# Kernel optimization log

Measured on AMD Instinct MI355X. Metric: run time of the kernel, lower is better.

## Reference

```python
import jax, jax.numpy as jnp
import numpy as np

N = 100000          # nodes
E = 1600000         # edges
F = 128             # input features
H = 128             # hidden_channels
G = 64              # graphs in batch


def setup_inputs() -> dict:
    key = jax.random.key(0)
    ks = jax.random.split(key, 16)
    x = jax.random.normal(ks[0], (N, F), dtype=jnp.float32)
    edge_index = jax.random.randint(ks[1], (2, E), 0, N, dtype=jnp.int32)
    batch = jnp.sort(jax.random.randint(ks[2], (N,), 0, G, dtype=jnp.int32))

    def glorot(k, fan_in, fan_out):
        s = jnp.sqrt(6.0 / (fan_in + fan_out)).astype(jnp.float32)
        return jax.random.uniform(k, (fan_in, fan_out), jnp.float32, -s, s)

    return {
        "x": x, "edge_index": edge_index, "batch": batch,
        "W1": glorot(ks[3], F, H),       "b1": jnp.zeros((H,), jnp.float32),
        "W2": glorot(ks[4], H, H),       "b2": jnp.zeros((H,), jnp.float32),
        "W3": glorot(ks[5], H, 2 * H),   "b3": jnp.zeros((2 * H,), jnp.float32),
        "W4": glorot(ks[6], 2 * H, H),   "b4": jnp.zeros((H,), jnp.float32),
        "Wl": glorot(ks[7], F, H),       "bl": jnp.zeros((H,), jnp.float32),
    }


def _gcn_conv(x, W, b, src, dst, deg_inv_sqrt):
    # PyG GCNConv: add self-loops, symmetric normalization D^-1/2 (A+I) D^-1/2
    h = x @ W                                  # [N, out]
    norm = deg_inv_sqrt[src] * deg_inv_sqrt[dst]      # [E]
    msg = h[src] * norm[:, None]               # gather + scale, [E, out]
    agg = jax.ops.segment_sum(msg, dst, num_segments=N)
    agg = agg + h * (deg_inv_sqrt * deg_inv_sqrt)[:, None]  # self-loop term (norm = 1/deg)
    return agg + b


def reference(x, edge_index, batch, W1, b1, W2, b2, W3, b3, W4, b4, Wl, bl):
    src, dst = edge_index[0], edge_index[1]
    # degree (incl. self-loop) from dst, as in PyG gcn_norm
    deg = jax.ops.segment_sum(jnp.ones((E,), jnp.float32), dst, num_segments=N) + 1.0
    deg_inv_sqrt = jax.lax.rsqrt(deg)

    identity = x
    x = jax.nn.relu(_gcn_conv(x, W1, b1, src, dst, deg_inv_sqrt))
    x = jax.nn.relu(_gcn_conv(x, W2, b2, src, dst, deg_inv_sqrt))
    x = jax.nn.relu(_gcn_conv(x, W3, b3, src, dst, deg_inv_sqrt))
    x = _gcn_conv(x, W4, b4, src, dst, deg_inv_sqrt)
    x = x + (identity @ Wl + bl)

    # global_mean_pool over graph ids
    sums = jax.ops.segment_sum(x, batch, num_segments=G)
    cnts = jax.ops.segment_sum(jnp.ones((N,), jnp.float32), batch, num_segments=G)
    return sums / jnp.maximum(cnts, 1.0)[:, None]
```

## Files before the change

kernel.cpp:

```cpp
#include <hip/hip_runtime.h>

#define NN 100000
#define EE 1600000
#define GG 64
#define PBLK 391
#define PCHUNK 4096
#define NBUCK 196

typedef __attribute__((ext_vector_type(8))) short short8v;
typedef __attribute__((ext_vector_type(4))) float f32x4;

__device__ __forceinline__ unsigned short f2bf(float f) {
    unsigned u = __float_as_uint(f);
    u = (u + 0x7FFFu + ((u >> 16) & 1)) >> 16;
    return (unsigned short)u;
}
__device__ __forceinline__ float bf2f(unsigned short s) {
    return __uint_as_float((unsigned)s << 16);
}

__global__ __launch_bounds__(256) void partitionA_kernel(const int* __restrict__ src,
                                                         const int* __restrict__ dst,
                                                         int* __restrict__ cnt,
                                                         int* __restrict__ ghist,
                                                         int* __restrict__ gboff,
                                                         int2* __restrict__ stage) {
    __shared__ int hist[NBUCK];
    __shared__ int boff[NBUCK];
    __shared__ int bcur[NBUCK];
    int b = blockIdx.x, t = threadIdx.x;
    int e0 = b * PCHUNK;
    int n = EE - e0;
    if (n > PCHUNK) n = PCHUNK;
    for (int i = t; i < NBUCK; i += 256) { hist[i] = 0; bcur[i] = 0; }
    __syncthreads();
    for (int i = t; i < n; i += 256) {
        int d = dst[e0 + i];
        atomicAdd(&cnt[d], 1);
        atomicAdd(&hist[d >> 9], 1);
    }
    __syncthreads();
    if (t == 0) {
        int run = 0;
        for (int k = 0; k < NBUCK; ++k) { boff[k] = run; run += hist[k]; }
    }
    __syncthreads();
    for (int i = t; i < n; i += 256) {
        int d = dst[e0 + i];
        int sv = src[e0 + i];
        int k = d >> 9;
        int p = boff[k] + atomicAdd(&bcur[k], 1);
        stage[(size_t)b * PCHUNK + p] = make_int2(sv, d);
    }
    for (int k = t; k < NBUCK; k += 256) {
        ghist[b * NBUCK + k] = hist[k];
        gboff[b * NBUCK + k] = boff[k];
    }
}

__global__ __launch_bounds__(256) void dis_kernel(const int* __restrict__ cnt,
                                                  float* __restrict__ dis) {
    int i = blockIdx.x * 256 + threadIdx.x;
    if (i < NN) dis[i] = rsqrtf((float)cnt[i] + 1.0f);
}

#define SCAN_EPB 1024
__global__ __launch_bounds__(256) void scan_block_kernel(const int* __restrict__ in,
                                                         int* __restrict__ out,
                                                         int* __restrict__ bsums) {
    __shared__ int sd[256];
    int t = threadIdx.x;
    int base = blockIdx.x * SCAN_EPB + t * 4;
    int v[4];
#pragma unroll
    for (int j = 0; j < 4; ++j) v[j] = (base + j < NN) ? in[base + j] : 0;
    int s = v[0] + v[1] + v[2] + v[3];
    sd[t] = s;
    __syncthreads();
    for (int off = 1; off < 256; off <<= 1) {
        int add = (t >= off) ? sd[t - off] : 0;
        __syncthreads();
        sd[t] += add;
        __syncthreads();
    }
    int ex = sd[t] - s;
    int run = ex;
#pragma unroll
    for (int j = 0; j < 4; ++j) {
        if (base + j < NN) out[base + j] = run;
        run += v[j];
    }
    if (t == 255) bsums[blockIdx.x] = sd[255];
}

__global__ void scan_sums_kernel(int* __restrict__ bsums, int nb) {
    if (threadIdx.x == 0 && blockIdx.x == 0) {
        int run = 0;
        for (int i = 0; i < nb; ++i) {
            int v = bsums[i];
            bsums[i] = run;
            run += v;
        }
    }
}

__global__ __launch_bounds__(256) void scan_add_kernel(int* __restrict__ rs,
                                                       const int* __restrict__ bsums,
                                                       int* __restrict__ cursor) {
    int i = blockIdx.x * 256 + threadIdx.x;
    if (i < NN) {
        int v = rs[i] + bsums[i >> 10];
        rs[i] = v;
        cursor[i] = v;
    }
    if (i == 0) rs[NN] = EE;
}

__global__ __launch_bounds__(256) void scatterC_kernel(const int2* __restrict__ stage,
                                                       const int* __restrict__ ghist,
                                                       const int* __restrict__ gboff,
                                                       int* __restrict__ cursor,
                                                       int* __restrict__ csr) {
    int k = blockIdx.x;
    for (int b = threadIdx.x; b < PBLK; b += 256) {
        int c_ = ghist[b * NBUCK + k];
        size_t base = (size_t)b * PCHUNK + gboff[b * NBUCK + k];
        for (int i = 0; i < c_; ++i) {
            int2 e = stage[base + i];
            int p = atomicAdd(&cursor[e.y], 1);
            csr[p] = e.x;
        }
    }
}

__global__ __launch_bounds__(256) void cvt_kernel(const float* __restrict__ x,
                                                  const float* __restrict__ dis,
                                                  unsigned short* __restrict__ xb) {
    size_t i = ((size_t)blockIdx.x * 256 + threadIdx.x) * 8;
    float d = dis[i >> 7];
    float4 a = *(const float4*)(x + i);
    float4 b = *(const float4*)(x + i + 4);
    short8v v;
    v[0] = (short)f2bf(a.x * d); v[1] = (short)f2bf(a.y * d);
    v[2] = (short)f2bf(a.z * d); v[3] = (short)f2bf(a.w * d);
    v[4] = (short)f2bf(b.x * d); v[5] = (short)f2bf(b.y * d);
    v[6] = (short)f2bf(b.z * d); v[7] = (short)f2bf(b.w * d);
    *(short8v*)(xb + i) = v;
}

template <int K, int M>
__global__ __launch_bounds__(64) void packw_kernel(const float* __restrict__ W,
                                                   unsigned short* __restrict__ Wp) {
    const int NKS = K / 32;
    int ct = blockIdx.x / NKS, ks = blockIdx.x % NKS;
    int lane = threadIdx.x;
    int col = ct * 16 + (lane & 15);
    int kb = ks * 32 + (lane >> 4) * 8;
    unsigned short* o = Wp + ((size_t)(ct * NKS + ks) * 64 + lane) * 16;
#pragma unroll
    for (int i = 0; i < 8; ++i) {
        float f = W[(size_t)(kb + i) * M + col];
        unsigned short h = f2bf(f);
        unsigned short l = f2bf(f - bf2f(h));
        o[i] = h;
        o[8 + i] = l;
    }
}

template <int K, int M, int RT, bool ASPLIT, bool RELU, bool BIAS, bool ACCUM, bool DSCALE>
__global__ __launch_bounds__(256) void gemm_kernel(const void* __restrict__ Ain,
                                                   const unsigned short* __restrict__ Wp,
                                                   const float* __restrict__ bias,
                                                   const float* __restrict__ dis,
                                                   void* __restrict__ out) {
    const int NKS = K / 32;
    int tid = threadIdx.x;
    int wave = tid >> 6, lane = tid & 63;
    int r0 = blockIdx.x * (RT * 64) + wave * (RT * 16);

    short8v ah[RT][NKS];
    short8v al[ASPLIT ? RT : 1][ASPLIT ? NKS : 1];
#pragma unroll
    for (int t = 0; t < RT; ++t) {
        int ra = r0 + t * 16 + (lane & 15);
        if (ra > NN - 1) ra = NN - 1;
        if (ASPLIT) {
            const float* A = (const float*)Ain;
#pragma unroll
            for (int ks = 0; ks < NKS; ++ks) {
                const float* p = A + (size_t)ra * K + ks * 32 + (lane >> 4) * 8;
                float4 v0 = *(const float4*)p;
                float4 v1 = *(const float4*)(p + 4);
                float f[8] = {v0.x, v0.y, v0.z, v0.w, v1.x, v1.y, v1.z, v1.w};
#pragma unroll
                for (int i = 0; i < 8; ++i) {
                    unsigned short h = f2bf(f[i]);
                    ah[t][ks][i] = (short)h;
                    al[t][ks][i] = (short)f2bf(f[i] - bf2f(h));
                }
            }
        } else {
            const unsigned short* A = (const unsigned short*)Ain;
#pragma unroll
            for (int ks = 0; ks < NKS; ++ks)
                ah[t][ks] = *(const short8v*)(A + (size_t)ra * K + ks * 32 + (lane >> 4) * 8);
        }
    }

    float dsc[RT][4];
#pragma unroll
    for (int t = 0; t < RT; ++t)
#pragma unroll
        for (int i = 0; i < 4; ++i) {
            int row = r0 + t * 16 + (lane >> 4) * 4 + i;
            dsc[t][i] = (DSCALE && row < NN) ? dis[row] : 1.f;
        }

#pragma unroll
    for (int ct = 0; ct < 8; ++ct) {
        int ctg = blockIdx.y * 8 + ct;
        int col = ctg * 16 + (lane & 15);
        float bv = BIAS ? bias[col] : 0.f;
        f32x4 acc[RT];
#pragma unroll
        for (int t = 0; t < RT; ++t) {
            acc[t][0] = bv; acc[t][1] = bv; acc[t][2] = bv; acc[t][3] = bv;
        }
#pragma unroll
        for (int ks = 0; ks < NKS; ++ks) {
            const short8v* pW = (const short8v*)Wp + ((size_t)(ctg * NKS + ks) * 64 + lane) * 2;
            short8v bh = pW[0], blo = pW[1];
#pragma unroll
            for (int t = 0; t < RT; ++t) {
                acc[t] = __builtin_amdgcn_mfma_f32_16x16x32_bf16(ah[t][ks], bh, acc[t], 0, 0, 0);
                acc[t] = __builtin_amdgcn_mfma_f32_16x16x32_bf16(ah[t][ks], blo, acc[t], 0, 0, 0);
                if (ASPLIT)
                    acc[t] = __builtin_amdgcn_mfma_f32_16x16x32_bf16(al[t][ks], bh, acc[t], 0, 0, 0);
            }
        }
#pragma unroll
        for (int t = 0; t < RT; ++t)
#pragma unroll
            for (int i = 0; i < 4; ++i) {
                int row = r0 + t * 16 + (lane >> 4) * 4 + i;
                if (row >= NN) continue;
                float v = acc[t][i];
                if (RELU) v = fmaxf(v, 0.f);
                if (ACCUM) {
                    ((float*)out)[(size_t)row * M + col] += v;
                } else {
                    ((unsigned short*)out)[(size_t)row * M + col] = f2bf(v * dsc[t][i]);
                }
            }
    }
}

template <int OUTMODE>
__global__ __launch_bounds__(256) void aggb_kernel(const unsigned short* __restrict__ h,
                                                   const float* __restrict__ dis,
                                                   const int* __restrict__ csr,
                                                   const int* __restrict__ rs,
                                                   const float* __restrict__ bias,
                                                   void* __restrict__ out) {
    int node = blockIdx.x * 4 + (threadIdx.x >> 6);
    int lane = threadIdx.x & 63;
    if (node >= NN) return;
    int c = lane & 15;
    int s = lane >> 4;
    int beg = rs[node], end = rs[node + 1];
    const uint4* hb = (const uint4*)h;
    float acc[8] = {};
    for (int e0 = beg; e0 < end; e0 += 32) {
        uint4 v[8];
#pragma unroll
        for (int j = 0; j < 8; ++j) {
            v[j] = make_uint4(0u, 0u, 0u, 0u);
            int ej = e0 + j * 4 + s;
            if (ej < end) v[j] = hb[(size_t)csr[ej] * 16 + c];
        }
#pragma unroll
        for (int j = 0; j < 8; ++j) {
            acc[0] += __uint_as_float(v[j].x << 16);
            acc[1] += __uint_as_float(v[j].x & 0xFFFF0000u);
            acc[2] += __uint_as_float(v[j].y << 16);
            acc[3] += __uint_as_float(v[j].y & 0xFFFF0000u);
            acc[4] += __uint_as_float(v[j].z << 16);
            acc[5] += __uint_as_float(v[j].z & 0xFFFF0000u);
            acc[6] += __uint_as_float(v[j].w << 16);
            acc[7] += __uint_as_float(v[j].w & 0xFFFF0000u);
        }
    }
#pragma unroll
    for (int i = 0; i < 8; ++i) {
        acc[i] += __shfl_xor(acc[i], 16, 64);
        acc[i] += __shfl_xor(acc[i], 32, 64);
    }
    if (s == 0) {
        float d = dis[node];
        uint4 us = hb[(size_t)node * 16 + c];
        float sf[8];
        sf[0] = __uint_as_float(us.x << 16); sf[1] = __uint_as_float(us.x & 0xFFFF0000u);
        sf[2] = __uint_as_float(us.y << 16); sf[3] = __uint_as_float(us.y & 0xFFFF0000u);
        sf[4] = __uint_as_float(us.z << 16); sf[5] = __uint_as_float(us.z & 0xFFFF0000u);
        sf[6] = __uint_as_float(us.w << 16); sf[7] = __uint_as_float(us.w & 0xFFFF0000u);
        float r[8];
#pragma unroll
        for (int i = 0; i < 8; ++i) r[i] = d * (acc[i] + sf[i]);
        if (OUTMODE == 0) {
            uint4 o;
            o.x = (unsigned)f2bf(r[0]) | ((unsigned)f2bf(r[1]) << 16);
            o.y = (unsigned)f2bf(r[2]) | ((unsigned)f2bf(r[3]) << 16);
            o.z = (unsigned)f2bf(r[4]) | ((unsigned)f2bf(r[5]) << 16);
            o.w = (unsigned)f2bf(r[6]) | ((unsigned)f2bf(r[7]) << 16);
            ((uint4*)out)[(size_t)node * 16 + c] = o;
        } else {
#pragma unroll
            for (int i = 0; i < 8; ++i) r[i] += bias[c * 8 + i];
            float4 o0 = make_float4(r[0], r[1], r[2], r[3]);
            float4 o1 = make_float4(r[4], r[5], r[6], r[7]);
            float* O = (float*)out + (size_t)node * 128 + c * 8;
            *(float4*)O = o0;
            *(float4*)(O + 4) = o1;
        }
    }
}

__global__ __launch_bounds__(128) void pool_partial_kernel(const float* __restrict__ y,
                                                           const int* __restrict__ batch,
                                                           float* __restrict__ P) {
    int c = threadIdx.x;
    int chunk = (NN + gridDim.x - 1) / gridDim.x;
    int n0 = blockIdx.x * chunk;
    int n1 = n0 + chunk;
    if (n1 > NN) n1 = NN;
    if (n0 >= NN) return;
    int curg = batch[n0];
    float acc = 0.f;
    for (int n = n0; n < n1; ++n) {
        int g = batch[n];
        if (g != curg) {
            atomicAdd(&P[curg * 128 + c], acc);
            acc = 0.f;
            curg = g;
        }
        acc += y[(size_t)n * 128 + c];
    }
    atomicAdd(&P[curg * 128 + c], acc);
}

__global__ __launch_bounds__(128) void pool_final_kernel(const float* __restrict__ P,
                                                         const int* __restrict__ batch,
                                                         float* __restrict__ out) {
    int g = blockIdx.x, c = threadIdx.x;
    int lo = 0, hi = NN;
    while (lo < hi) {
        int m = (lo + hi) >> 1;
        if (batch[m] < g) lo = m + 1;
        else hi = m;
    }
    int start = lo;
    int lo2 = start, hi2 = NN;
    while (lo2 < hi2) {
        int m = (lo2 + hi2) >> 1;
        if (batch[m] < g + 1) lo2 = m + 1;
        else hi2 = m;
    }
    float cntg = (float)(lo2 - start);
    out[g * 128 + c] = P[g * 128 + c] / fmaxf(cntg, 1.f);
}

extern "C" void kernel_launch(void* const* d_in, const int* in_sizes, int n_in,
                              void* d_out, int out_size, void* d_ws, size_t ws_size,
                              hipStream_t stream) {
    const float* x = (const float*)d_in[0];
    const int* ei = (const int*)d_in[1];
    const int* batch = (const int*)d_in[2];
    const float* W1 = (const float*)d_in[3];
    const float* b1 = (const float*)d_in[4];
    const float* W2 = (const float*)d_in[5];
    const float* b2 = (const float*)d_in[6];
    const float* W3 = (const float*)d_in[7];
    const float* b3 = (const float*)d_in[8];
    const float* W4 = (const float*)d_in[9];
    const float* b4 = (const float*)d_in[10];
    const float* Wl = (const float*)d_in[11];
    const float* bl = (const float*)d_in[12];
    float* out = (float*)d_out;

    char* p = (char*)d_ws;
    auto alloc = [&](size_t bytes) {
        void* r = (void*)p;
        p += (bytes + 255) & ~(size_t)255;
        return r;
    };
    int* cnt = (int*)alloc((size_t)NN * 4);
    int* rs = (int*)alloc((size_t)(NN + 1) * 4);
    int* cursor = (int*)alloc((size_t)NN * 4);
    float* dis = (float*)alloc((size_t)NN * 4);
    const int NB = (NN + SCAN_EPB - 1) / SCAN_EPB;
    int* bsums = (int*)alloc((size_t)NB * 4);
    int* csr = (int*)alloc((size_t)EE * 4);
    int* ghist = (int*)alloc((size_t)PBLK * NBUCK * 4);
    int* gboff = (int*)alloc((size_t)PBLK * NBUCK * 4);
    unsigned short* xb = (unsigned short*)alloc((size_t)NN * 128 * 2);
    unsigned short* AG = (unsigned short*)alloc((size_t)NN * 128 * 2);
    unsigned short* GM = (unsigned short*)alloc((size_t)NN * 128 * 2);
    unsigned short* H3 = (unsigned short*)alloc((size_t)NN * 256 * 2);
    float* Y = (float*)alloc((size_t)NN * 128 * 4);
    unsigned short* W1p = (unsigned short*)alloc(8 * 4 * 64 * 16 * 2);
    unsigned short* W2p = (unsigned short*)alloc(8 * 4 * 64 * 16 * 2);
    unsigned short* W3p = (unsigned short*)alloc(16 * 4 * 64 * 16 * 2);
    unsigned short* W4p = (unsigned short*)alloc(8 * 8 * 64 * 16 * 2);
    unsigned short* Wlp = (unsigned short*)alloc(8 * 4 * 64 * 16 * 2);
    float* P = (float*)alloc((size_t)GG * 128 * 4);
    int2* stage = (int2*)Y;

    const int* src = ei;
    const int* dst = ei + EE;

    hipMemsetAsync(cnt, 0, (size_t)NN * 4, stream);
    hipMemsetAsync(P, 0, (size_t)GG * 128 * 4, stream);

    partitionA_kernel<<<PBLK, 256, 0, stream>>>(src, dst, cnt, ghist, gboff, stage);
    dis_kernel<<<(NN + 255) / 256, 256, 0, stream>>>(cnt, dis);
    cvt_kernel<<<(NN * 128) / (256 * 8), 256, 0, stream>>>(x, dis, xb);
    scan_block_kernel<<<NB, 256, 0, stream>>>(cnt, rs, bsums);
    scan_sums_kernel<<<1, 64, 0, stream>>>(bsums, NB);
    scan_add_kernel<<<(NN + 255) / 256, 256, 0, stream>>>(rs, bsums, cursor);
    scatterC_kernel<<<NBUCK, 256, 0, stream>>>(stage, ghist, gboff, cursor, csr);

    packw_kernel<128, 128><<<8 * 4, 64, 0, stream>>>(W1, W1p);
    packw_kernel<128, 128><<<8 * 4, 64, 0, stream>>>(W2, W2p);
    packw_kernel<128, 256><<<16 * 4, 64, 0, stream>>>(W3, W3p);
    packw_kernel<256, 128><<<8 * 8, 64, 0, stream>>>(W4, W4p);
    packw_kernel<128, 128><<<8 * 4, 64, 0, stream>>>(Wl, Wlp);

    const int AGG_GRID = (NN + 3) / 4;
    const int GX4 = (NN + 255) / 256;
    const int GX2 = (NN + 127) / 128;

    aggb_kernel<0><<<AGG_GRID, 256, 0, stream>>>(xb, dis, csr, rs, nullptr, AG);
    gemm_kernel<128, 128, 4, false, true, true, false, true><<<dim3(GX4, 1), 256, 0, stream>>>(AG, W1p, b1, dis, GM);
    aggb_kernel<0><<<AGG_GRID, 256, 0, stream>>>(GM, dis, csr, rs, nullptr, AG);
    gemm_kernel<128, 128, 4, false, true, true, false, true><<<dim3(GX4, 1), 256, 0, stream>>>(AG, W2p, b2, dis, GM);
    aggb_kernel<0><<<AGG_GRID, 256, 0, stream>>>(GM, dis, csr, rs, nullptr, AG);
    gemm_kernel<128, 256, 4, false, true, true, false, false><<<dim3(GX4, 2), 256, 0, stream>>>(AG, W3p, b3, nullptr, H3);
    gemm_kernel<256, 128, 2, false, false, false, false, true><<<dim3(GX2, 1), 256, 0, stream>>>(H3, W4p, nullptr, dis, AG);
    aggb_kernel<1><<<AGG_GRID, 256, 0, stream>>>(AG, dis, csr, rs, b4, Y);
    gemm_kernel<128, 128, 2, true, false, true, true, false><<<dim3(GX2, 1), 256, 0, stream>>>(x, Wlp, bl, nullptr, Y);
    pool_partial_kernel<<<512, 128, 0, stream>>>(Y, batch, P);
    pool_final_kernel<<<GG, 128, 0, stream>>>(P, batch, out);
}
```

Before: 844.2 us.

## Shrink partition chunks, parallel-scan bucket offsets, 2D scatter grid, shuffle CSR indices

Partition chunks shrink from 4096 to 1024 edges, so there are more blocks. Each thread keeps its src/dst values in registers instead of reloading them. The serial single-thread bucket prefix sum is replaced by a shared-memory Hillis-Steele scan. The scatter kernel gets a 2D grid so each thread handles exactly one chunk per bucket, and the aggregation kernel loads 32 CSR indices once per wavefront and broadcasts them with shuffles instead of reloading them per lane. The aim is to cut serialization in graph preprocessing and redundant index loads in aggregation, at the cost of more blocks and extra atomics contention on the cursor array.

```diff
diff --git a/kernel.cpp b/kernel.cpp
--- a/kernel.cpp
+++ b/kernel.cpp
@@ -3,8 +3,8 @@
 #define NN 100000
 #define EE 1600000
 #define GG 64
-#define PBLK 391
-#define PCHUNK 4096
+#define PCHUNK 1024
+#define PBLK 1563
 #define NBUCK 196
 
 typedef __attribute__((ext_vector_type(8))) short short8v;
@@ -26,35 +26,49 @@
                                                          int* __restrict__ gboff,
                                                          int2* __restrict__ stage) {
     __shared__ int hist[NBUCK];
+    __shared__ int sc[256];
     __shared__ int boff[NBUCK];
     __shared__ int bcur[NBUCK];
     int b = blockIdx.x, t = threadIdx.x;
     int e0 = b * PCHUNK;
     int n = EE - e0;
     if (n > PCHUNK) n = PCHUNK;
-    for (int i = t; i < NBUCK; i += 256) { hist[i] = 0; bcur[i] = 0; }
+    if (t < NBUCK) { hist[t] = 0; bcur[t] = 0; }
     __syncthreads();
-    for (int i = t; i < n; i += 256) {
-        int d = dst[e0 + i];
-        atomicAdd(&cnt[d], 1);
-        atomicAdd(&hist[d >> 9], 1);
+    int dv[4], sv[4];
+#pragma unroll
+    for (int j = 0; j < 4; ++j) {
+        int i = t + j * 256;
+        if (i < n) {
+            dv[j] = dst[e0 + i];
+            sv[j] = src[e0 + i];
+            atomicAdd(&cnt[dv[j]], 1);
+            atomicAdd(&hist[dv[j] >> 9], 1);
+        }
     }
     __syncthreads();
-    if (t == 0) {
-        int run = 0;
-        for (int k = 0; k < NBUCK; ++k) { boff[k] = run; run += hist[k]; }
-    }
+    sc[t] = (t < NBUCK) ? hist[t] : 0;
     __syncthreads();
-    for (int i = t; i < n; i += 256) {
-        int d = dst[e0 + i];
-        int sv = src[e0 + i];
-        int k = d >> 9;
-        int p = boff[k] + atomicAdd(&bcur[k], 1);
-        stage[(size_t)b * PCHUNK + p] = make_int2(sv, d);
-    }
-    for (int k = t; k < NBUCK; k += 256) {
-        ghist[b * NBUCK + k] = hist[k];
-        gboff[b * NBUCK + k] = boff[k];
+    for (int off = 1; off < 256; off <<= 1) {
+        int a = (t >= off) ? sc[t - off] : 0;
+        __syncthreads();
+        sc[t] += a;
+        __syncthreads();
+    }
+    if (t < NBUCK) boff[t] = sc[t] - hist[t];
+    __syncthreads();
+#pragma unroll
+    for (int j = 0; j < 4; ++j) {
+        int i = t + j * 256;
+        if (i < n) {
+            int k = dv[j] >> 9;
+            int p = boff[k] + atomicAdd(&bcur[k], 1);
+            stage[(size_t)b * PCHUNK + p] = make_int2(sv[j], dv[j]);
+        }
+    }
+    if (t < NBUCK) {
+        ghist[b * NBUCK + t] = hist[t];
+        gboff[b * NBUCK + t] = boff[t];
     }
 }
 
@@ -122,14 +136,14 @@
                                                        int* __restrict__ cursor,
                                                        int* __restrict__ csr) {
     int k = blockIdx.x;
-    for (int b = threadIdx.x; b < PBLK; b += 256) {
-        int c_ = ghist[b * NBUCK + k];
-        size_t base = (size_t)b * PCHUNK + gboff[b * NBUCK + k];
-        for (int i = 0; i < c_; ++i) {
-            int2 e = stage[base + i];
-            int p = atomicAdd(&cursor[e.y], 1);
-            csr[p] = e.x;
-        }
+    int b = blockIdx.y * 256 + threadIdx.x;
+    if (b >= PBLK) return;
+    int c_ = ghist[b * NBUCK + k];
+    size_t base = (size_t)b * PCHUNK + gboff[b * NBUCK + k];
+    for (int i = 0; i < c_; ++i) {
+        int2 e = stage[base + i];
+        int p = atomicAdd(&cursor[e.y], 1);
+        csr[p] = e.x;
     }
 }
 
@@ -271,12 +285,16 @@
     const uint4* hb = (const uint4*)h;
     float acc[8] = {};
     for (int e0 = beg; e0 < end; e0 += 32) {
+        int myidx = 0;
+        int el = e0 + lane;
+        if (lane < 32 && el < end) myidx = csr[el];
         uint4 v[8];
 #pragma unroll
         for (int j = 0; j < 8; ++j) {
+            int sidx = __shfl(myidx, j * 4 + s, 64);
             v[j] = make_uint4(0u, 0u, 0u, 0u);
             int ej = e0 + j * 4 + s;
-            if (ej < end) v[j] = hb[(size_t)csr[ej] * 16 + c];
+            if (ej < end) v[j] = hb[(size_t)sidx * 16 + c];
         }
 #pragma unroll
         for (int j = 0; j < 8; ++j) {
@@ -427,7 +445,7 @@
     scan_block_kernel<<<NB, 256, 0, stream>>>(cnt, rs, bsums);
     scan_sums_kernel<<<1, 64, 0, stream>>>(bsums, NB);
     scan_add_kernel<<<(NN + 255) / 256, 256, 0, stream>>>(rs, bsums, cursor);
-    scatterC_kernel<<<NBUCK, 256, 0, stream>>>(stage, ghist, gboff, cursor, csr);
+    scatterC_kernel<<<dim3(NBUCK, (PBLK + 255) / 256), 256, 0, stream>>>(stage, ghist, gboff, cursor, csr);
 
     packw_kernel<128, 128><<<8 * 4, 64, 0, stream>>>(W1, W1p);
     packw_kernel<128, 128><<<8 * 4, 64, 0, stream>>>(W2, W2p);
```

New measurement: 798.4 us. 5.4% less time.
